# Optimization experiments

Measured on AMD Instinct MI355X. Metric: run time of the kernel, lower is better.

Reference implementation:

```python
import jax, jax.numpy as jnp
import numpy as np

N = 16384        # num particles (nodes)
E = 65536        # num edges (avg degree 4)
C = 32           # channels
IC = 64          # inter_channels
K = 16           # kernel taps = 4*4
EPS = 1e-5       # haiku BatchNorm default eps


def _conv_params(key, c_in, c_out):
    k1, k2 = jax.random.split(key)
    W = jax.random.normal(k1, (K, c_in, c_out), jnp.float32) / np.sqrt(K * c_in)
    P = jax.random.normal(k2, (3, K), jnp.float32)   # rel_pos -> kernel tap logits
    b = jnp.zeros((c_out,), jnp.float32)
    return W, P, b


def _bn_params(key, dim):
    k1, k2 = jax.random.split(key)
    scale = jnp.ones((dim,), jnp.float32)
    offset = jnp.zeros((dim,), jnp.float32)
    mean = 0.1 * jax.random.normal(k1, (dim,), jnp.float32)
    var = jax.random.uniform(k2, (dim,), jnp.float32, 0.5, 1.5)
    return scale, offset, mean, var


def setup_inputs() -> dict:
    key = jax.random.key(0)
    ks = jax.random.split(key, 16)
    d = {}
    d['x'] = jax.random.normal(ks[0], (N, C), jnp.float32)
    d['y'] = jax.random.normal(ks[1], (N, C), jnp.float32)
    d['senders'] = jax.random.randint(ks[2], (E,), 0, N)
    d['receivers'] = jax.random.randint(ks[3], (E,), 0, N)
    d['rel_pos'] = jax.random.normal(ks[4], (E, 3), jnp.float32)
    d['a'] = jax.random.uniform(ks[5], (E,), jnp.float32)
    dims = [(2 * C, IC), (IC, C), (C, IC), (IC, C)]
    for i, (ci, co) in enumerate(dims, start=1):
        W, P, b = _conv_params(ks[5 + i], ci, co)
        d[f'W{i}'], d[f'P{i}'], d[f'b{i}'] = W, P, b
        s, o, m, v = _bn_params(ks[9 + i], co)
        d[f's{i}'], d[f'o{i}'], d[f'm{i}'], d[f'v{i}'] = s, o, m, v
    return d


def _cconv(feat, senders, receivers, rel_pos, a, W, P, b):
    # Continuous conv: gather sender features, interpolate K kernel taps
    # from rel_pos, per-edge contraction, weight by a, scatter-add to receivers.
    fe = feat[senders]                                  # (E, Cin) gather
    w = jax.nn.softmax(rel_pos @ P, axis=-1)            # (E, K) tap weights
    fw = fe[:, None, :] * w[:, :, None]                 # (E, K, Cin)
    oe = jnp.einsum('eki,kio->eo', fw, W) * a[:, None]  # (E, Cout)
    return jax.ops.segment_sum(oe, receivers, num_segments=N) + b


def _bn(h, scale, offset, mean, var):
    # haiku BatchNorm, is_training=False (moving-average stats)
    return (h - mean) * jax.lax.rsqrt(var + EPS) * scale + offset


def reference(x, y, rel_pos, a,
              W1, P1, b1, s1, o1, m1, v1,
              W2, P2, b2, s2, o2, m2, v2,
              W3, P3, b3, s3, o3, m3, v3,
              W4, P4, b4, s4, o4, m4, v4,
              senders, receivers):
    xa = jnp.concatenate([x, y], axis=-1)               # (N, 2C)
    xl = _cconv(xa, senders, receivers, rel_pos, a, W1, P1, b1)
    xl = jax.nn.relu(_bn(xl, s1, o1, m1, v1))
    xl = _cconv(xl, senders, receivers, rel_pos, a, W2, P2, b2)
    xl = _bn(xl, s2, o2, m2, v2)
    wei1 = jax.nn.sigmoid(xl)
    xo = 2.0 * x * wei1 + 2.0 * y * (1.0 - wei1)        # first AFF fusion
    xl2 = _cconv(xo, senders, receivers, rel_pos, a, W3, P3, b3)
    xl2 = jax.nn.relu(_bn(xl2, s3, o3, m3, v3))
    xl2 = _cconv(xl2, senders, receivers, rel_pos, a, W4, P4, b4)
    xl2 = _bn(xl2, s4, o4, m4, v4)
    wei2 = jax.nn.sigmoid(xl2)
    return 2.0 * x * wei2 + 2.0 * y * (1.0 - wei2)      # second AFF fusion
```

## Files before the change

### kernel.cpp

```cpp
#include <hip/hip_runtime.h>
#include <hip/hip_bf16.h>

#define NN 16384
#define NE 65536

typedef __attribute__((ext_vector_type(8))) short short8;
typedef __attribute__((ext_vector_type(4))) float f32x4;

using bf16 = __hip_bfloat16;

__device__ __forceinline__ float b2f(bf16 v){ return __bfloat162float(v); }
__device__ __forceinline__ bf16 f2b(float v){ return __float2bfloat16(v); }

__global__ __launch_bounds__(256) void k_init(
    unsigned* __restrict__ curs,
    const float* __restrict__ rel, const float* __restrict__ a,
    const float* __restrict__ P1, const float* __restrict__ P2,
    const float* __restrict__ P3, const float* __restrict__ P4,
    float* __restrict__ g,
    const float* __restrict__ W1, const float* __restrict__ W2,
    const float* __restrict__ W3, const float* __restrict__ W4,
    bf16* __restrict__ Bp)
{
    int b = blockIdx.x;
    if(b < 64){
        curs[b*256 + threadIdx.x] = 0u;
        return;
    }
    if(b < 320){
        int e = (b-64)*256 + threadIdx.x;
        float r0 = rel[e*3+0], r1 = rel[e*3+1], r2 = rel[e*3+2];
        float av = a[e];
        const float* Ps[4] = {P1,P2,P3,P4};
        for(int c=0;c<4;c++){
            const float* P = Ps[c];
            float lg[16]; float mx = -1e30f;
            #pragma unroll
            for(int k=0;k<16;k++){
                float v = r0*P[k] + r1*P[16+k] + r2*P[32+k];
                lg[k] = v; mx = fmaxf(mx, v);
            }
            float ssum = 0.f;
            #pragma unroll
            for(int k=0;k<16;k++){ lg[k] = __expf(lg[k]-mx); ssum += lg[k]; }
            float inv = av/ssum;
            float* go = &g[((size_t)c*NE + e)*16];
            #pragma unroll
            for(int j=0;j<4;j++){
                ((float4*)go)[j] = make_float4(lg[j*4]*inv, lg[j*4+1]*inv,
                                               lg[j*4+2]*inv, lg[j*4+3]*inv);
            }
        }
        return;
    }
    int t = (b-320)*256 + threadIdx.x;
    const float* W; int Cout; int base; int tl;
    if(t < 8192)      { W=W1; Cout=64; base=0;     tl=t; }
    else if(t < 12288){ W=W2; Cout=32; base=8192;  tl=t-8192; }
    else if(t < 16384){ W=W3; Cout=64; base=12288; tl=t-12288; }
    else              { W=W4; Cout=32; base=16384; tl=t-16384; }
    int l  = tl & 63;
    int NCT = Cout >> 4;
    int ct = (tl >> 6) % NCT;
    int ks = (tl >> 6) / NCT;
    int col = ct*16 + (l & 15);
    int k0  = ks*32 + ((l >> 4) & 3)*8;
    short8 v;
    #pragma unroll
    for(int j=0;j<8;j++){
        bf16 h = f2b(W[(size_t)(k0+j)*Cout + col]);
        v[j] = (short)*(unsigned short*)&h;
    }
    ((short8*)Bp)[base + tl] = v;
}

__global__ __launch_bounds__(256) void k_countfill(const int* __restrict__ recv,
                                                   const int* __restrict__ send,
                                                   unsigned* __restrict__ curs,
                                                   unsigned* __restrict__ csr){
    int e = blockIdx.x*256 + threadIdx.x;
    if(e >= NE) return;
    int rv = recv[e];
    unsigned pos = atomicAdd(&curs[rv], 1u);
    if(pos < 32u) csr[(unsigned)rv*32u + pos] = ((unsigned)e << 14) | (unsigned)send[e];
}

template<int CIN, int NCT, int MODE, bool CONCAT, typename OT>
__global__ __launch_bounds__(1024, 4) void k_conv(
    const void* __restrict__ fAv, const float* __restrict__ fBv,
    const float* __restrict__ g,
    const unsigned* __restrict__ csr, const unsigned* __restrict__ curs,
    const bf16* __restrict__ Bp, const float* __restrict__ bias,
    const float* __restrict__ bns, const float* __restrict__ bno,
    const float* __restrict__ bnm, const float* __restrict__ bnv,
    const float* __restrict__ x, const float* __restrict__ y,
    OT* __restrict__ out)
{
    constexpr int KD   = CIN*16;
    constexpr int ROWB = KD*2;
    __shared__ __align__(16) char sT[16*ROWB];
    int wv = threadIdx.x >> 6, lane = threadIdx.x & 63;
    int nbase = blockIdx.x*16;
    int node  = nbase + wv;
    int nl    = wv;

    const float* fAf = (const float*)fAv;
    const bf16*  fAb = (const bf16*)fAv;
    const int i     = (CIN==64) ? lane : (lane & 31);
    const int kbase = (CIN==64) ? 0 : ((lane >> 5) * 8);
    unsigned cnt = curs[node]; if(cnt > 32u) cnt = 32u;
    const unsigned* crow = csr + (unsigned)node*32u;
    uint4 ca = ((const uint4*)crow)[0];
    uint4 cb = ((const uint4*)crow)[1];
    unsigned uu[8] = {ca.x, ca.y, ca.z, ca.w, cb.x, cb.y, cb.z, cb.w};

    constexpr int KPL = (CIN==64) ? 16 : 8;
    float acc[KPL];
    #pragma unroll
    for(int r=0;r<KPL;r++) acc[r] = 0.f;

    auto edge = [&](unsigned u){
        int sid = (int)(u & 16383u);
        int eid = (int)(u >> 14);
        float fe;
        if(CONCAT){
            fe = (lane < 32) ? fAf[sid*32 + lane] : fBv[sid*32 + (lane-32)];
        } else {
            fe = b2f(fAb[sid*CIN + i]);
        }
        const float4* gp = (const float4*)&g[(size_t)eid*16 + kbase];
        if(CIN==64){
            float4 g0=gp[0], g1=gp[1], g2=gp[2], g3=gp[3];
            acc[0]  += g0.x*fe; acc[1]  += g0.y*fe; acc[2]  += g0.z*fe; acc[3]  += g0.w*fe;
            acc[4]  += g1.x*fe; acc[5]  += g1.y*fe; acc[6]  += g1.z*fe; acc[7]  += g1.w*fe;
            acc[8]  += g2.x*fe; acc[9]  += g2.y*fe; acc[10] += g2.z*fe; acc[11] += g2.w*fe;
            acc[12] += g3.x*fe; acc[13] += g3.y*fe; acc[14] += g3.z*fe; acc[15] += g3.w*fe;
        } else {
            float4 g0=gp[0], g1=gp[1];
            acc[0] += g0.x*fe; acc[1] += g0.y*fe; acc[2] += g0.z*fe; acc[3] += g0.w*fe;
            acc[4] += g1.x*fe; acc[5] += g1.y*fe; acc[6] += g1.z*fe; acc[7] += g1.w*fe;
        }
    };
    #pragma unroll
    for(int j=0;j<8;j++){
        if((unsigned)j < cnt) edge(uu[j]);
    }
    for(unsigned j=8; j<cnt; j++) edge(crow[j]);

    unsigned xo_ = (unsigned)((nl & 7) << 4);
    if(CIN==64){
        #pragma unroll
        for(int k=0;k<16;k++){
            unsigned byte = (unsigned)nl*ROWB + ((((unsigned)(k*64 + lane))*2u) ^ xo_);
            *(bf16*)(sT + byte) = f2b(acc[k]);
        }
    } else {
        #pragma unroll
        for(int r=0;r<8;r++){
            unsigned byte = (unsigned)nl*ROWB + ((((unsigned)((kbase+r)*32 + i))*2u) ^ xo_);
            *(bf16*)(sT + byte) = f2b(acc[r]);
        }
    }
    __syncthreads();

    if(wv >= NCT) return;
    int r = lane & 15, h = lane >> 4;
    int c = wv;
    const short8* Bp8 = (const short8*)Bp;
    f32x4 acc4 = (f32x4){0.f,0.f,0.f,0.f};
    unsigned xr = (unsigned)((r & 7) << 4);
    #pragma unroll 8
    for(int ks=0; ks<KD/32; ks++){
        unsigned ab = (unsigned)r*ROWB + (((unsigned)(ks*64 + h*16)) ^ xr);
        short8 af  = *(const short8*)(sT + ab);
        short8 bfr = Bp8[(ks*NCT + c)*64 + lane];
        acc4 = __builtin_amdgcn_mfma_f32_16x16x32_bf16(af, bfr, acc4, 0, 0, 0);
    }

    const int Cout = NCT*16;
    int col = c*16 + r;
    float inv = rsqrtf(bnv[col] + 1e-5f);
    float al  = bns[col] * inv;
    float be  = al*(bias[col] - bnm[col]) + bno[col];
    #pragma unroll
    for(int j=0;j<4;j++){
        int rr = nbase + h*4 + j;
        float v = al*acc4[j] + be;
        if(MODE==0){
            out[(size_t)rr*Cout + col] = (OT)fmaxf(v, 0.f);
        } else {
            float wei = 1.f/(1.f + __expf(-v));
            float xv = x[rr*32 + col];
            float yv = y[rr*32 + col];
            out[(size_t)rr*32 + col] = (OT)(2.f*xv*wei + 2.f*yv*(1.f - wei));
        }
    }
}

extern "C" void kernel_launch(void* const* d_in, const int* in_sizes, int n_in,
                              void* d_out, int out_size, void* d_ws, size_t ws_size,
                              hipStream_t stream){
    const float* x   = (const float*)d_in[0];
    const float* y   = (const float*)d_in[1];
    const int* send  = (const int*)d_in[2];
    const int* recv  = (const int*)d_in[3];
    const float* rel = (const float*)d_in[4];
    const float* a   = (const float*)d_in[5];
    const float *W[4], *P[4], *bb[4], *bs[4], *bo[4], *bm[4], *bv[4];
    for(int i=0;i<4;i++){
        int base = 6 + i*7;
        W[i]  = (const float*)d_in[base+0];
        P[i]  = (const float*)d_in[base+1];
        bb[i] = (const float*)d_in[base+2];
        bs[i] = (const float*)d_in[base+3];
        bo[i] = (const float*)d_in[base+4];
        bm[i] = (const float*)d_in[base+5];
        bv[i] = (const float*)d_in[base+6];
    }
    char* w = (char*)d_ws;
    float*    g    = (float*)(w);
    unsigned* curs = (unsigned*)(w + 16777216);
    unsigned* csr  = (unsigned*)(w + 16842752);
    bf16*     h1   = (bf16*)(w + 18939904);
    bf16*     xo   = (bf16*)(w + 21037056);
    bf16*     h3   = (bf16*)(w + 22085632);
    bf16*     Bp   = (bf16*)(w + 24182784);
    float*    outp = (float*)d_out;

    k_init     <<<400, 256, 0, stream>>>(curs, rel, a, P[0], P[1], P[2], P[3], g,
                                         W[0], W[1], W[2], W[3], Bp);
    k_countfill<<<NE/256, 256, 0, stream>>>(recv, send, curs, csr);

    (k_conv<64,4,0,true,bf16>)  <<<NN/16, 1024, 0, stream>>>(x, y, g + (size_t)0*NE*16, csr, curs,
        Bp + (size_t)0*8,     bb[0], bs[0], bo[0], bm[0], bv[0], nullptr, nullptr, h1);
    (k_conv<64,2,1,false,bf16>) <<<NN/16, 1024, 0, stream>>>(h1, nullptr, g + (size_t)1*NE*16, csr, curs,
        Bp + (size_t)8192*8,  bb[1], bs[1], bo[1], bm[1], bv[1], x, y, xo);
    (k_conv<32,4,0,false,bf16>) <<<NN/16, 1024, 0, stream>>>(xo, nullptr, g + (size_t)2*NE*16, csr, curs,
        Bp + (size_t)12288*8, bb[2], bs[2], bo[2], bm[2], bv[2], nullptr, nullptr, h3);
    (k_conv<64,2,1,false,float>)<<<NN/16, 1024, 0, stream>>>(h3, nullptr, g + (size_t)3*NE*16, csr, curs,
        Bp + (size_t)16384*8, bb[3], bs[3], bo[3], bm[3], bv[3], x, y, outp);
}
```

Before: 98.34 us.

## Process two nodes per wave in conv kernels and fuse CSR build into setup

Each wave now gathers edges for two nodes with interleaved accumulators, so a block covers 32 nodes and more waves take part in the MFMA stage. This raises memory-level parallelism in the gather and halves the grid size. The count/fill kernel is merged into the tap-weight setup kernel, and the cursor zeroing moves to a hipMemsetAsync, which removes one kernel launch. The costs are doubled register pressure per lane and twice the LDS per block, which may reduce occupancy.

```diff
diff --git a/kernel.cpp b/kernel.cpp
--- a/kernel.cpp
+++ b/kernel.cpp
@@ -12,8 +12,9 @@
 __device__ __forceinline__ float b2f(bf16 v){ return __bfloat162float(v); }
 __device__ __forceinline__ bf16 f2b(float v){ return __float2bfloat16(v); }
 
-__global__ __launch_bounds__(256) void k_init(
-    unsigned* __restrict__ curs,
+__global__ __launch_bounds__(256) void k_setup(
+    const int* __restrict__ recv, const int* __restrict__ send,
+    unsigned* __restrict__ curs, unsigned* __restrict__ csr,
     const float* __restrict__ rel, const float* __restrict__ a,
     const float* __restrict__ P1, const float* __restrict__ P2,
     const float* __restrict__ P3, const float* __restrict__ P4,
@@ -23,12 +24,11 @@
     bf16* __restrict__ Bp)
 {
     int b = blockIdx.x;
-    if(b < 64){
-        curs[b*256 + threadIdx.x] = 0u;
-        return;
-    }
-    if(b < 320){
-        int e = (b-64)*256 + threadIdx.x;
+    if(b < 256){
+        int e = b*256 + threadIdx.x;
+        int rv = recv[e];
+        unsigned pos = atomicAdd(&curs[rv], 1u);
+        if(pos < 32u) csr[(unsigned)rv*32u + pos] = ((unsigned)e << 14) | (unsigned)send[e];
         float r0 = rel[e*3+0], r1 = rel[e*3+1], r2 = rel[e*3+2];
         float av = a[e];
         const float* Ps[4] = {P1,P2,P3,P4};
@@ -53,7 +53,7 @@
         }
         return;
     }
-    int t = (b-320)*256 + threadIdx.x;
+    int t = (b-256)*256 + threadIdx.x;
     const float* W; int Cout; int base; int tl;
     if(t < 8192)      { W=W1; Cout=64; base=0;     tl=t; }
     else if(t < 12288){ W=W2; Cout=32; base=8192;  tl=t-8192; }
@@ -72,17 +72,6 @@
         v[j] = (short)*(unsigned short*)&h;
     }
     ((short8*)Bp)[base + tl] = v;
-}
-
-__global__ __launch_bounds__(256) void k_countfill(const int* __restrict__ recv,
-                                                   const int* __restrict__ send,
-                                                   unsigned* __restrict__ curs,
-                                                   unsigned* __restrict__ csr){
-    int e = blockIdx.x*256 + threadIdx.x;
-    if(e >= NE) return;
-    int rv = recv[e];
-    unsigned pos = atomicAdd(&curs[rv], 1u);
-    if(pos < 32u) csr[(unsigned)rv*32u + pos] = ((unsigned)e << 14) | (unsigned)send[e];
 }
 
 template<int CIN, int NCT, int MODE, bool CONCAT, typename OT>
@@ -98,28 +87,30 @@
 {
     constexpr int KD   = CIN*16;
     constexpr int ROWB = KD*2;
-    __shared__ __align__(16) char sT[16*ROWB];
+    __shared__ __align__(16) char sT[32*ROWB];
     int wv = threadIdx.x >> 6, lane = threadIdx.x & 63;
-    int nbase = blockIdx.x*16;
-    int node  = nbase + wv;
-    int nl    = wv;
+    int nbase = blockIdx.x*32;
+    int nA = nbase + wv*2, nB = nA + 1;
 
     const float* fAf = (const float*)fAv;
     const bf16*  fAb = (const bf16*)fAv;
     const int i     = (CIN==64) ? lane : (lane & 31);
     const int kbase = (CIN==64) ? 0 : ((lane >> 5) * 8);
-    unsigned cnt = curs[node]; if(cnt > 32u) cnt = 32u;
-    const unsigned* crow = csr + (unsigned)node*32u;
-    uint4 ca = ((const uint4*)crow)[0];
-    uint4 cb = ((const uint4*)crow)[1];
-    unsigned uu[8] = {ca.x, ca.y, ca.z, ca.w, cb.x, cb.y, cb.z, cb.w};
+    unsigned cntA = curs[nA]; if(cntA > 32u) cntA = 32u;
+    unsigned cntB = curs[nB]; if(cntB > 32u) cntB = 32u;
+    const unsigned* crA = csr + (unsigned)nA*32u;
+    const unsigned* crB = csr + (unsigned)nB*32u;
+    uint4 a0 = ((const uint4*)crA)[0], a1 = ((const uint4*)crA)[1];
+    uint4 b0 = ((const uint4*)crB)[0], b1 = ((const uint4*)crB)[1];
+    unsigned uA[8] = {a0.x, a0.y, a0.z, a0.w, a1.x, a1.y, a1.z, a1.w};
+    unsigned uB[8] = {b0.x, b0.y, b0.z, b0.w, b1.x, b1.y, b1.z, b1.w};
 
     constexpr int KPL = (CIN==64) ? 16 : 8;
-    float acc[KPL];
-    #pragma unroll
-    for(int r=0;r<KPL;r++) acc[r] = 0.f;
-
-    auto edge = [&](unsigned u){
+    float accA[KPL], accB[KPL];
+    #pragma unroll
+    for(int r=0;r<KPL;r++){ accA[r] = 0.f; accB[r] = 0.f; }
+
+    auto edge = [&](unsigned u, float* acc){
         int sid = (int)(u & 16383u);
         int eid = (int)(u >> 14);
         float fe;
@@ -143,35 +134,45 @@
     };
     #pragma unroll
     for(int j=0;j<8;j++){
-        if((unsigned)j < cnt) edge(uu[j]);
-    }
-    for(unsigned j=8; j<cnt; j++) edge(crow[j]);
-
-    unsigned xo_ = (unsigned)((nl & 7) << 4);
-    if(CIN==64){
-        #pragma unroll
-        for(int k=0;k<16;k++){
-            unsigned byte = (unsigned)nl*ROWB + ((((unsigned)(k*64 + lane))*2u) ^ xo_);
-            *(bf16*)(sT + byte) = f2b(acc[k]);
-        }
-    } else {
-        #pragma unroll
-        for(int r=0;r<8;r++){
-            unsigned byte = (unsigned)nl*ROWB + ((((unsigned)((kbase+r)*32 + i))*2u) ^ xo_);
-            *(bf16*)(sT + byte) = f2b(acc[r]);
+        if((unsigned)j < cntA) edge(uA[j], accA);
+        if((unsigned)j < cntB) edge(uB[j], accB);
+    }
+    for(unsigned j=8; j<cntA; j++) edge(crA[j], accA);
+    for(unsigned j=8; j<cntB; j++) edge(crB[j], accB);
+
+    {
+        int nlA = wv*2, nlB = wv*2+1;
+        unsigned xA = (unsigned)((nlA & 7) << 4);
+        unsigned xB = (unsigned)((nlB & 7) << 4);
+        if(CIN==64){
+            #pragma unroll
+            for(int k=0;k<16;k++){
+                unsigned off = (unsigned)(k*64 + lane)*2u;
+                *(bf16*)(sT + (unsigned)nlA*ROWB + (off ^ xA)) = f2b(accA[k]);
+                *(bf16*)(sT + (unsigned)nlB*ROWB + (off ^ xB)) = f2b(accB[k]);
+            }
+        } else {
+            #pragma unroll
+            for(int r=0;r<8;r++){
+                unsigned off = (unsigned)((kbase+r)*32 + i)*2u;
+                *(bf16*)(sT + (unsigned)nlA*ROWB + (off ^ xA)) = f2b(accA[r]);
+                *(bf16*)(sT + (unsigned)nlB*ROWB + (off ^ xB)) = f2b(accB[r]);
+            }
         }
     }
     __syncthreads();
 
-    if(wv >= NCT) return;
+    if(wv >= 2*NCT) return;
+    int rt, c;
+    if(NCT==4){ rt = wv >> 2; c = wv & 3; }
+    else      { rt = wv >> 1; c = wv & 1; }
     int r = lane & 15, h = lane >> 4;
-    int c = wv;
     const short8* Bp8 = (const short8*)Bp;
     f32x4 acc4 = (f32x4){0.f,0.f,0.f,0.f};
     unsigned xr = (unsigned)((r & 7) << 4);
     #pragma unroll 8
     for(int ks=0; ks<KD/32; ks++){
-        unsigned ab = (unsigned)r*ROWB + (((unsigned)(ks*64 + h*16)) ^ xr);
+        unsigned ab = (unsigned)(rt*16 + r)*ROWB + (((unsigned)(ks*64 + h*16)) ^ xr);
         short8 af  = *(const short8*)(sT + ab);
         short8 bfr = Bp8[(ks*NCT + c)*64 + lane];
         acc4 = __builtin_amdgcn_mfma_f32_16x16x32_bf16(af, bfr, acc4, 0, 0, 0);
@@ -184,7 +185,7 @@
     float be  = al*(bias[col] - bnm[col]) + bno[col];
     #pragma unroll
     for(int j=0;j<4;j++){
-        int rr = nbase + h*4 + j;
+        int rr = nbase + rt*16 + h*4 + j;
         float v = al*acc4[j] + be;
         if(MODE==0){
             out[(size_t)rr*Cout + col] = (OT)fmaxf(v, 0.f);
@@ -227,16 +228,17 @@
     bf16*     Bp   = (bf16*)(w + 24182784);
     float*    outp = (float*)d_out;
 
-    k_init     <<<400, 256, 0, stream>>>(curs, rel, a, P[0], P[1], P[2], P[3], g,
-                                         W[0], W[1], W[2], W[3], Bp);
-    k_countfill<<<NE/256, 256, 0, stream>>>(recv, send, curs, csr);
-
-    (k_conv<64,4,0,true,bf16>)  <<<NN/16, 1024, 0, stream>>>(x, y, g + (size_t)0*NE*16, csr, curs,
+    hipMemsetAsync(curs, 0, NN*sizeof(unsigned), stream);
+    k_setup<<<336, 256, 0, stream>>>(recv, send, curs, csr, rel, a,
+                                     P[0], P[1], P[2], P[3], g,
+                                     W[0], W[1], W[2], W[3], Bp);
+
+    (k_conv<64,4,0,true,bf16>)  <<<NN/32, 1024, 0, stream>>>(x, y, g + (size_t)0*NE*16, csr, curs,
         Bp + (size_t)0*8,     bb[0], bs[0], bo[0], bm[0], bv[0], nullptr, nullptr, h1);
-    (k_conv<64,2,1,false,bf16>) <<<NN/16, 1024, 0, stream>>>(h1, nullptr, g + (size_t)1*NE*16, csr, curs,
+    (k_conv<64,2,1,false,bf16>) <<<NN/32, 1024, 0, stream>>>(h1, nullptr, g + (size_t)1*NE*16, csr, curs,
         Bp + (size_t)8192*8,  bb[1], bs[1], bo[1], bm[1], bv[1], x, y, xo);
-    (k_conv<32,4,0,false,bf16>) <<<NN/16, 1024, 0, stream>>>(xo, nullptr, g + (size_t)2*NE*16, csr, curs,
+    (k_conv<32,4,0,false,bf16>) <<<NN/32, 1024, 0, stream>>>(xo, nullptr, g + (size_t)2*NE*16, csr, curs,
         Bp + (size_t)12288*8, bb[2], bs[2], bo[2], bm[2], bv[2], nullptr, nullptr, h3);
-    (k_conv<64,2,1,false,float>)<<<NN/16, 1024, 0, stream>>>(h3, nullptr, g + (size_t)3*NE*16, csr, curs,
+    (k_conv<64,2,1,false,float>)<<<NN/32, 1024, 0, stream>>>(h3, nullptr, g + (size_t)3*NE*16, csr, curs,
         Bp + (size_t)16384*8, bb[3], bs[3], bo[3], bm[3], bv[3], x, y, outp);
 }
```

Result: slower. 101.3 us (+3.0%).

## Fuse CSR build into setup kernel, precast x/y to bf16, widen edge prefetch

Applied to the files above, without the earlier changes.

Moves the counter reset to a memset and folds the CSR count/fill into the setup kernel alongside the tap-weight and weight-packing work, removing one kernel launch. Adds a conversion pass that writes concatenated x|y as bf16, so the first conv gathers half-width bf16 features instead of branching between two fp32 arrays. The conv kernel now preloads 12 CSR entries instead of 8, and its launch-bounds occupancy hint goes from 4 to 8. Risks: register pressure under the tighter bound, extra precision loss on the first layer input, and atomics now sharing a kernel with the heavier softmax work.

```diff
diff --git a/kernel.cpp b/kernel.cpp
--- a/kernel.cpp
+++ b/kernel.cpp
@@ -12,23 +12,25 @@
 __device__ __forceinline__ float b2f(bf16 v){ return __bfloat162float(v); }
 __device__ __forceinline__ bf16 f2b(float v){ return __float2bfloat16(v); }
 
-__global__ __launch_bounds__(256) void k_init(
-    unsigned* __restrict__ curs,
+__global__ __launch_bounds__(256) void k_setup(
+    const int* __restrict__ recv, const int* __restrict__ send,
+    unsigned* __restrict__ curs, unsigned* __restrict__ csr,
     const float* __restrict__ rel, const float* __restrict__ a,
     const float* __restrict__ P1, const float* __restrict__ P2,
     const float* __restrict__ P3, const float* __restrict__ P4,
     float* __restrict__ g,
     const float* __restrict__ W1, const float* __restrict__ W2,
     const float* __restrict__ W3, const float* __restrict__ W4,
-    bf16* __restrict__ Bp)
+    bf16* __restrict__ Bp,
+    const float* __restrict__ x, const float* __restrict__ y,
+    bf16* __restrict__ xyc)
 {
     int b = blockIdx.x;
-    if(b < 64){
-        curs[b*256 + threadIdx.x] = 0u;
-        return;
-    }
-    if(b < 320){
-        int e = (b-64)*256 + threadIdx.x;
+    if(b < 256){
+        int e = b*256 + threadIdx.x;
+        int rv = recv[e];
+        unsigned pos = atomicAdd(&curs[rv], 1u);
+        if(pos < 32u) csr[(unsigned)rv*32u + pos] = ((unsigned)e << 14) | (unsigned)send[e];
         float r0 = rel[e*3+0], r1 = rel[e*3+1], r2 = rel[e*3+2];
         float av = a[e];
         const float* Ps[4] = {P1,P2,P3,P4};
@@ -53,41 +55,53 @@
         }
         return;
     }
-    int t = (b-320)*256 + threadIdx.x;
-    const float* W; int Cout; int base; int tl;
-    if(t < 8192)      { W=W1; Cout=64; base=0;     tl=t; }
-    else if(t < 12288){ W=W2; Cout=32; base=8192;  tl=t-8192; }
-    else if(t < 16384){ W=W3; Cout=64; base=12288; tl=t-12288; }
-    else              { W=W4; Cout=32; base=16384; tl=t-16384; }
-    int l  = tl & 63;
-    int NCT = Cout >> 4;
-    int ct = (tl >> 6) % NCT;
-    int ks = (tl >> 6) / NCT;
-    int col = ct*16 + (l & 15);
-    int k0  = ks*32 + ((l >> 4) & 3)*8;
-    short8 v;
-    #pragma unroll
-    for(int j=0;j<8;j++){
-        bf16 h = f2b(W[(size_t)(k0+j)*Cout + col]);
-        v[j] = (short)*(unsigned short*)&h;
-    }
-    ((short8*)Bp)[base + tl] = v;
+    if(b < 336){
+        int t = (b-256)*256 + threadIdx.x;
+        const float* W; int Cout; int base; int tl;
+        if(t < 8192)      { W=W1; Cout=64; base=0;     tl=t; }
+        else if(t < 12288){ W=W2; Cout=32; base=8192;  tl=t-8192; }
+        else if(t < 16384){ W=W3; Cout=64; base=12288; tl=t-12288; }
+        else              { W=W4; Cout=32; base=16384; tl=t-16384; }
+        int l  = tl & 63;
+        int NCT = Cout >> 4;
+        int ct = (tl >> 6) % NCT;
+        int ks = (tl >> 6) / NCT;
+        int col = ct*16 + (l & 15);
+        int k0  = ks*32 + ((l >> 4) & 3)*8;
+        short8 v;
+        #pragma unroll
+        for(int j=0;j<8;j++){
+            bf16 h = f2b(W[(size_t)(k0+j)*Cout + col]);
+            v[j] = (short)*(unsigned short*)&h;
+        }
+        ((short8*)Bp)[base + tl] = v;
+        return;
+    }
+    int t = (b-336)*256 + threadIdx.x;
+    int n = t >> 1, half = t & 1;
+    const float* src = half ? (y + n*32) : (x + n*32);
+    bf16* dst = xyc + (size_t)n*64 + half*32;
+    #pragma unroll
+    for(int j=0;j<4;j++){
+        float4 v0 = ((const float4*)src)[2*j];
+        float4 v1 = ((const float4*)src)[2*j+1];
+        short8 o;
+        bf16 h;
+        h = f2b(v0.x); o[0]=(short)*(unsigned short*)&h;
+        h = f2b(v0.y); o[1]=(short)*(unsigned short*)&h;
+        h = f2b(v0.z); o[2]=(short)*(unsigned short*)&h;
+        h = f2b(v0.w); o[3]=(short)*(unsigned short*)&h;
+        h = f2b(v1.x); o[4]=(short)*(unsigned short*)&h;
+        h = f2b(v1.y); o[5]=(short)*(unsigned short*)&h;
+        h = f2b(v1.z); o[6]=(short)*(unsigned short*)&h;
+        h = f2b(v1.w); o[7]=(short)*(unsigned short*)&h;
+        ((short8*)dst)[j] = o;
+    }
 }
 
-__global__ __launch_bounds__(256) void k_countfill(const int* __restrict__ recv,
-                                                   const int* __restrict__ send,
-                                                   unsigned* __restrict__ curs,
-                                                   unsigned* __restrict__ csr){
-    int e = blockIdx.x*256 + threadIdx.x;
-    if(e >= NE) return;
-    int rv = recv[e];
-    unsigned pos = atomicAdd(&curs[rv], 1u);
-    if(pos < 32u) csr[(unsigned)rv*32u + pos] = ((unsigned)e << 14) | (unsigned)send[e];
-}
-
-template<int CIN, int NCT, int MODE, bool CONCAT, typename OT>
-__global__ __launch_bounds__(1024, 4) void k_conv(
-    const void* __restrict__ fAv, const float* __restrict__ fBv,
+template<int CIN, int NCT, int MODE, typename OT>
+__global__ __launch_bounds__(1024, 8) void k_conv(
+    const bf16* __restrict__ fAb,
     const float* __restrict__ g,
     const unsigned* __restrict__ csr, const unsigned* __restrict__ curs,
     const bf16* __restrict__ Bp, const float* __restrict__ bias,
@@ -102,18 +116,16 @@
     int wv = threadIdx.x >> 6, lane = threadIdx.x & 63;
     int nbase = blockIdx.x*16;
     int node  = nbase + wv;
-    int nl    = wv;
-
-    const float* fAf = (const float*)fAv;
-    const bf16*  fAb = (const bf16*)fAv;
+
+    const unsigned* crow = csr + (unsigned)node*32u;
+    unsigned cnt = curs[node]; if(cnt > 32u) cnt = 32u;
+    uint4 c0 = ((const uint4*)crow)[0];
+    uint4 c1 = ((const uint4*)crow)[1];
+    uint4 c2 = ((const uint4*)crow)[2];
+    unsigned uu[12] = {c0.x,c0.y,c0.z,c0.w, c1.x,c1.y,c1.z,c1.w, c2.x,c2.y,c2.z,c2.w};
+
     const int i     = (CIN==64) ? lane : (lane & 31);
     const int kbase = (CIN==64) ? 0 : ((lane >> 5) * 8);
-    unsigned cnt = curs[node]; if(cnt > 32u) cnt = 32u;
-    const unsigned* crow = csr + (unsigned)node*32u;
-    uint4 ca = ((const uint4*)crow)[0];
-    uint4 cb = ((const uint4*)crow)[1];
-    unsigned uu[8] = {ca.x, ca.y, ca.z, ca.w, cb.x, cb.y, cb.z, cb.w};
-
     constexpr int KPL = (CIN==64) ? 16 : 8;
     float acc[KPL];
     #pragma unroll
@@ -122,12 +134,7 @@
     auto edge = [&](unsigned u){
         int sid = (int)(u & 16383u);
         int eid = (int)(u >> 14);
-        float fe;
-        if(CONCAT){
-            fe = (lane < 32) ? fAf[sid*32 + lane] : fBv[sid*32 + (lane-32)];
-        } else {
-            fe = b2f(fAb[sid*CIN + i]);
-        }
+        float fe = b2f(fAb[sid*CIN + i]);
         const float4* gp = (const float4*)&g[(size_t)eid*16 + kbase];
         if(CIN==64){
             float4 g0=gp[0], g1=gp[1], g2=gp[2], g3=gp[3];
@@ -142,22 +149,22 @@
         }
     };
     #pragma unroll
-    for(int j=0;j<8;j++){
+    for(int j=0;j<12;j++){
         if((unsigned)j < cnt) edge(uu[j]);
     }
-    for(unsigned j=8; j<cnt; j++) edge(crow[j]);
-
-    unsigned xo_ = (unsigned)((nl & 7) << 4);
+    for(unsigned j=12; j<cnt; j++) edge(crow[j]);
+
+    unsigned xo_ = (unsigned)((wv & 7) << 4);
     if(CIN==64){
         #pragma unroll
         for(int k=0;k<16;k++){
-            unsigned byte = (unsigned)nl*ROWB + ((((unsigned)(k*64 + lane))*2u) ^ xo_);
+            unsigned byte = (unsigned)wv*ROWB + ((((unsigned)(k*64 + lane))*2u) ^ xo_);
             *(bf16*)(sT + byte) = f2b(acc[k]);
         }
     } else {
         #pragma unroll
         for(int r=0;r<8;r++){
-            unsigned byte = (unsigned)nl*ROWB + ((((unsigned)((kbase+r)*32 + i))*2u) ^ xo_);
+            unsigned byte = (unsigned)wv*ROWB + ((((unsigned)((kbase+r)*32 + i))*2u) ^ xo_);
             *(bf16*)(sT + byte) = f2b(acc[r]);
         }
     }
@@ -225,18 +232,21 @@
     bf16*     xo   = (bf16*)(w + 21037056);
     bf16*     h3   = (bf16*)(w + 22085632);
     bf16*     Bp   = (bf16*)(w + 24182784);
+    bf16*     xyc  = (bf16*)(w + 24510464);
     float*    outp = (float*)d_out;
 
-    k_init     <<<400, 256, 0, stream>>>(curs, rel, a, P[0], P[1], P[2], P[3], g,
-                                         W[0], W[1], W[2], W[3], Bp);
-    k_countfill<<<NE/256, 256, 0, stream>>>(recv, send, curs, csr);
-
-    (k_conv<64,4,0,true,bf16>)  <<<NN/16, 1024, 0, stream>>>(x, y, g + (size_t)0*NE*16, csr, curs,
+    hipMemsetAsync(curs, 0, NN*sizeof(unsigned), stream);
+    k_setup<<<464, 256, 0, stream>>>(recv, send, curs, csr, rel, a,
+                                     P[0], P[1], P[2], P[3], g,
+                                     W[0], W[1], W[2], W[3], Bp,
+                                     x, y, xyc);
+
+    (k_conv<64,4,0,bf16>) <<<NN/16, 1024, 0, stream>>>(xyc, g + (size_t)0*NE*16, csr, curs,
         Bp + (size_t)0*8,     bb[0], bs[0], bo[0], bm[0], bv[0], nullptr, nullptr, h1);
-    (k_conv<64,2,1,false,bf16>) <<<NN/16, 1024, 0, stream>>>(h1, nullptr, g + (size_t)1*NE*16, csr, curs,
+    (k_conv<64,2,1,bf16>) <<<NN/16, 1024, 0, stream>>>(h1, g + (size_t)1*NE*16, csr, curs,
         Bp + (size_t)8192*8,  bb[1], bs[1], bo[1], bm[1], bv[1], x, y, xo);
-    (k_conv<32,4,0,false,bf16>) <<<NN/16, 1024, 0, stream>>>(xo, nullptr, g + (size_t)2*NE*16, csr, curs,
+    (k_conv<32,4,0,bf16>) <<<NN/16, 1024, 0, stream>>>(xo, g + (size_t)2*NE*16, csr, curs,
         Bp + (size_t)12288*8, bb[2], bs[2], bo[2], bm[2], bv[2], nullptr, nullptr, h3);
-    (k_conv<64,2,1,false,float>)<<<NN/16, 1024, 0, stream>>>(h3, nullptr, g + (size_t)3*NE*16, csr, curs,
+    (k_conv<64,2,1,float>)<<<NN/16, 1024, 0, stream>>>(h3, g + (size_t)3*NE*16, csr, curs,
         Bp + (size_t)16384*8, bb[3], bs[3], bo[3], bm[3], bv[3], x, y, outp);
 }
```

Result: no change. 99.70 us (+1.4%).
